# Optimization experiments

Measured on AMD Instinct MI355X. Metric: run time of the kernel, lower is better.

The kernel has to match this reference:

```python
import jax, jax.numpy as jnp
import numpy as np

N = 50000
E = 800000
D_IN = 128
D_OUT = 128


def setup_inputs() -> dict:
    key = jax.random.key(0)
    ks = jax.random.split(key, 12)
    x = jax.random.normal(ks[0], (N, D_IN), dtype=jnp.float32)
    W1 = jax.random.normal(ks[1], (D_IN, D_OUT), dtype=jnp.float32) * (1.0 / np.sqrt(D_IN))
    b1 = jnp.zeros((D_OUT,), dtype=jnp.float32)
    W2 = jax.random.normal(ks[2], (D_IN, D_OUT), dtype=jnp.float32) * (1.0 / np.sqrt(D_IN))
    b2 = jnp.zeros((D_OUT,), dtype=jnp.float32)
    # inverted-dropout masks, p=0.5 -> values in {0, 2}
    def mask(k):
        return jnp.where(jax.random.uniform(k, (N, D_IN)) < 0.5, 0.0, 2.0).astype(jnp.float32)
    mask_pos1 = mask(ks[3])
    mask_neg1 = mask(ks[4])
    mask_pos2 = mask(ks[5])
    mask_neg2 = mask(ks[6])
    edge_index1 = jax.random.randint(ks[7], (2, E), 0, N, dtype=jnp.int32)
    edge_index2 = jax.random.randint(ks[8], (2, E), 0, N, dtype=jnp.int32)
    perm1 = jax.random.permutation(ks[9], N).astype(jnp.int32)
    perm2 = jax.random.permutation(ks[10], N).astype(jnp.int32)
    return dict(x=x, W1=W1, b1=b1, W2=W2, b2=b2,
                mask_pos1=mask_pos1, mask_neg1=mask_neg1,
                mask_pos2=mask_pos2, mask_neg2=mask_neg2,
                edge_index1=edge_index1, edge_index2=edge_index2,
                perm1=perm1, perm2=perm2)


def gcn_conv(x, W, b, edge_index):
    """PyG GCNConv: add self-loops, symmetric normalization, then x@W aggregation + bias."""
    n = x.shape[0]
    xw = x @ W  # [N, D_OUT]
    loops = jnp.arange(n, dtype=edge_index.dtype)
    src = jnp.concatenate([edge_index[0], loops])
    dst = jnp.concatenate([edge_index[1], loops])
    deg = jax.ops.segment_sum(jnp.ones_like(dst, dtype=xw.dtype), dst, num_segments=n)
    dinv = jax.lax.rsqrt(jnp.maximum(deg, 1.0))  # deg >= 1 due to self-loops
    norm = dinv[src] * dinv[dst]                 # [E+N]
    msg = xw[src] * norm[:, None]                # [E+N, D_OUT]
    out = jax.ops.segment_sum(msg, dst, num_segments=n)
    return out + b


def _branch(x, W, b, edge_index, mask_pos, mask_neg, perm):
    pos_h = jax.nn.relu(gcn_conv(x * mask_pos, W, b, edge_index))
    neg_in = (x * mask_neg)[perm]
    neg_h = jax.nn.relu(gcn_conv(neg_in, W, b, edge_index))
    summary = jnp.mean(pos_h, axis=0, keepdims=True)  # [1, D_OUT]
    return pos_h, neg_h, summary


def reference(x, W1, b1, W2, b2, mask_pos1, mask_neg1, mask_pos2, mask_neg2,
              edge_index1, edge_index2, perm1, perm2):
    p1, n1, s1 = _branch(x, W1, b1, edge_index1, mask_pos1, mask_neg1, perm1)
    p2, n2, s2 = _branch(x, W2, b2, edge_index2, mask_pos2, mask_neg2, perm2)
    return (p1, n1, s1, p2, n2, s2)
```

## Files before the change

kernel.cpp:

```cpp
#include <hip/hip_runtime.h>
#include <hip/hip_fp16.h>

#define NN 50000
#define NE 800000
#define D 128
#define NB 196
#define FILL_BLOCKS 1024
#define GEMM_BLOCKS 3128
#define RNG 6250
#define BCAP 131072

typedef _Float16 half8_t __attribute__((ext_vector_type(8)));
typedef _Float16 half4_t __attribute__((ext_vector_type(4)));
typedef float f32x4 __attribute__((ext_vector_type(4)));

__global__ void k_init(int* cnt1, int* cnt2, float* s1, float* s2, int* bcnt) {
    int i = blockIdx.x * blockDim.x + threadIdx.x;
    int stride = gridDim.x * blockDim.x;
    for (int j = i; j < NN; j += stride) { cnt1[j] = 0; cnt2[j] = 0; }
    if (i < D) { s1[i] = 0.f; s2[i] = 0.f; }
    if (i < 16) bcnt[i] = 0;
}

__global__ void k_bucket(const int* __restrict__ src1, const int* __restrict__ dst1,
                         const int* __restrict__ src2, const int* __restrict__ dst2,
                         int* bcnt,
                         int* bs1, int* bd1, int* bs2, int* bd2) {
    __shared__ int lcnt[16], lpos[16], gbase[16];
    int t = threadIdx.x;
    if (t < 16) { lcnt[t] = 0; lpos[t] = 0; }
    __syncthreads();

    int e0 = blockIdx.x * 256 + t;
    int s1v0=0,d1v0=0,s2v0=0,d2v0=0, s1v1=0,d1v1=0,s2v1=0,d2v1=0;
    int s1v2=0,d1v2=0,s2v2=0,d2v2=0, s1v3=0,d1v3=0,s2v3=0,d2v3=0;
    bool v0 = (e0 + 0 * 262144) < NE;
    bool v1 = (e0 + 1 * 262144) < NE;
    bool v2 = (e0 + 2 * 262144) < NE;
    bool v3 = (e0 + 3 * 262144) < NE;
    if (v0) { int e = e0;             s1v0 = src1[e]; d1v0 = dst1[e]; s2v0 = src2[e]; d2v0 = dst2[e]; }
    if (v1) { int e = e0 + 262144;    s1v1 = src1[e]; d1v1 = dst1[e]; s2v1 = src2[e]; d2v1 = dst2[e]; }
    if (v2) { int e = e0 + 2*262144;  s1v2 = src1[e]; d1v2 = dst1[e]; s2v2 = src2[e]; d2v2 = dst2[e]; }
    if (v3) { int e = e0 + 3*262144;  s1v3 = src1[e]; d1v3 = dst1[e]; s2v3 = src2[e]; d2v3 = dst2[e]; }

    if (v0) { atomicAdd(&lcnt[d1v0 / RNG], 1); atomicAdd(&lcnt[8 + d2v0 / RNG], 1); }
    if (v1) { atomicAdd(&lcnt[d1v1 / RNG], 1); atomicAdd(&lcnt[8 + d2v1 / RNG], 1); }
    if (v2) { atomicAdd(&lcnt[d1v2 / RNG], 1); atomicAdd(&lcnt[8 + d2v2 / RNG], 1); }
    if (v3) { atomicAdd(&lcnt[d1v3 / RNG], 1); atomicAdd(&lcnt[8 + d2v3 / RNG], 1); }
    __syncthreads();
    if (t < 16) gbase[t] = atomicAdd(&bcnt[t], lcnt[t]);
    __syncthreads();

    #define PLACE(sv, dv) { \
        int r = (dv) / RNG; \
        int p = gbase[r] + atomicAdd(&lpos[r], 1); \
        if (p < BCAP) { bs1[r * BCAP + p] = (sv); bd1[r * BCAP + p] = (dv); } }
    #define PLACE2(sv, dv) { \
        int r = (dv) / RNG; \
        int p = gbase[8 + r] + atomicAdd(&lpos[8 + r], 1); \
        if (p < BCAP) { bs2[r * BCAP + p] = (sv); bd2[r * BCAP + p] = (dv); } }
    if (v0) { PLACE(s1v0, d1v0); PLACE2(s2v0, d2v0); }
    if (v1) { PLACE(s1v1, d1v1); PLACE2(s2v1, d2v1); }
    if (v2) { PLACE(s1v2, d1v2); PLACE2(s2v2, d2v2); }
    if (v3) { PLACE(s1v3, d1v3); PLACE2(s2v3, d2v3); }
    #undef PLACE
    #undef PLACE2
}

__global__ void k_count_b(const int* __restrict__ bcnt,
                          const int* __restrict__ bd1, const int* __restrict__ bd2,
                          int* cnt1, int* cnt2) {
    int b = blockIdx.x & 7;
    int rank = blockIdx.x >> 3;
    int base = b * BCAP;
    int n1 = bcnt[b], n2 = bcnt[8 + b];
    for (int i = rank * 256 + threadIdx.x; i < n1; i += 32768)
        atomicAdd(&cnt1[bd1[base + i]], 1);
    for (int i = rank * 256 + threadIdx.x; i < n2; i += 32768)
        atomicAdd(&cnt2[bd2[base + i]], 1);
}

__global__ void k_part(const int* __restrict__ cnt1, const int* __restrict__ cnt2,
                       int* part1, int* part2) {
    __shared__ int sm1[256], sm2[256];
    int t = threadIdx.x;
    int idx = blockIdx.x * 256 + t;
    int v1 = (idx < NN) ? cnt1[idx] : 0;
    int v2 = (idx < NN) ? cnt2[idx] : 0;
    sm1[t] = v1; sm2[t] = v2;
    __syncthreads();
    for (int off = 128; off > 0; off >>= 1) {
        if (t < off) { sm1[t] += sm1[t + off]; sm2[t] += sm2[t + off]; }
        __syncthreads();
    }
    if (t == 0) { part1[blockIdx.x] = sm1[0]; part2[blockIdx.x] = sm2[0]; }
}

__global__ void k_scanp(int* part1, int* part2) {
    __shared__ int sm1[256], sm2[256];
    int t = threadIdx.x;
    int v1 = (t < NB) ? part1[t] : 0;
    int v2 = (t < NB) ? part2[t] : 0;
    sm1[t] = v1; sm2[t] = v2;
    __syncthreads();
    for (int off = 1; off < 256; off <<= 1) {
        int a1 = (t >= off) ? sm1[t - off] : 0;
        int a2 = (t >= off) ? sm2[t - off] : 0;
        __syncthreads();
        sm1[t] += a1; sm2[t] += a2;
        __syncthreads();
    }
    if (t < NB) { part1[t] = sm1[t] - v1; part2[t] = sm2[t] - v2; }
}

__global__ void k_apply(const int* __restrict__ cnt1, const int* __restrict__ cnt2,
                        const int* __restrict__ part1, const int* __restrict__ part2,
                        int* rp1, int* rp2, int* cur1, int* cur2,
                        float* dinv1, float* dinv2) {
    __shared__ int sm1[256], sm2[256];
    int b = blockIdx.x, t = threadIdx.x;
    int idx = b * 256 + t;
    int v1 = (idx < NN) ? cnt1[idx] : 0;
    int v2 = (idx < NN) ? cnt2[idx] : 0;
    sm1[t] = v1; sm2[t] = v2;
    __syncthreads();
    for (int off = 1; off < 256; off <<= 1) {
        int a1 = (t >= off) ? sm1[t - off] : 0;
        int a2 = (t >= off) ? sm2[t - off] : 0;
        __syncthreads();
        sm1[t] += a1; sm2[t] += a2;
        __syncthreads();
    }
    int e1 = sm1[t] - v1 + part1[b];
    int e2 = sm2[t] - v2 + part2[b];
    if (idx < NN) {
        rp1[idx] = e1; cur1[idx] = e1; dinv1[idx] = rsqrtf((float)(v1 + 1));
        rp2[idx] = e2; cur2[idx] = e2; dinv2[idx] = rsqrtf((float)(v2 + 1));
    } else if (idx == NN) {
        rp1[NN] = e1; rp2[NN] = e2;
    }
}

__launch_bounds__(256)
__global__ void k_fill_gemm(const int* __restrict__ bcnt,
                            const int* __restrict__ bs1, const int* __restrict__ bd1,
                            const int* __restrict__ bs2, const int* __restrict__ bd2,
                            int* cur1, int* cur2, int* col1, int* col2,
                            const float* __restrict__ x,
                            const float* __restrict__ W1, const float* __restrict__ W2,
                            const float* __restrict__ mp1, const float* __restrict__ mn1,
                            const float* __restrict__ mp2, const float* __restrict__ mn2,
                            const int* __restrict__ perm1, const int* __restrict__ perm2,
                            const float* __restrict__ dinv1, const float* __restrict__ dinv2,
                            _Float16* xwi1, _Float16* xwi2) {
    __shared__ __align__(16) _Float16 WT[128][136];
    int t = threadIdx.x;
    int bid = blockIdx.x;

    if (bid < FILL_BLOCKS) {
        int b = bid & 7;
        int rank = bid >> 3;
        int base = b * BCAP;
        int n1 = bcnt[b], n2 = bcnt[8 + b];
        for (int i = rank * 256 + t; i < n1; i += 32768) {
            int d = bd1[base + i];
            int p = atomicAdd(&cur1[d], 1);
            col1[p] = bs1[base + i];
        }
        for (int i = rank * 256 + t; i < n2; i += 32768) {
            int d = bd2[base + i];
            int p = atomicAdd(&cur2[d], 1);
            col2[p] = bs2[base + i];
        }
        return;
    }

    int g = bid - FILL_BLOCKS;
    int which = g / 782;
    int bx = g - which * 782;
    const float* W = (which < 2) ? W1 : W2;
    const float* mask = (which == 0) ? mp1 : (which == 1) ? mn1 : (which == 2) ? mp2 : mn2;
    const int* perm = (which == 1) ? perm1 : (which == 3) ? perm2 : nullptr;
    const float* dinv = (which < 2) ? dinv1 : dinv2;
    _Float16* out = ((which < 2) ? xwi1 : xwi2) + ((which & 1) ? 128 : 0);

    #pragma unroll
    for (int i = 0; i < 8; i++) {
        int idx = i * 256 + t;
        int j = idx & 127;
        int k0 = (idx >> 7) * 8;
        half8_t h;
        #pragma unroll
        for (int c = 0; c < 8; c++) h[c] = (_Float16)W[(k0 + c) * 128 + j];
        *(half8_t*)(&WT[j][k0]) = h;
    }
    __syncthreads();

    int wave = t >> 6;
    int lane = t & 63;
    int quad = lane >> 4;
    int m = lane & 15;
    int tile = bx * 4 + wave;
    bool active = (tile * 16 < NN);

    f32x4 accs[8];
    if (active) {
        int row = tile * 16 + m;
        int grow = perm ? perm[row] : row;
        const float* xrow = x + (long)grow * D;
        const float* mrow = mask + (long)grow * D;

        half8_t a[4];
        #pragma unroll
        for (int kk = 0; kk < 4; kk++) {
            int k0 = kk * 32 + quad * 8;
            float4 xa = *(const float4*)(xrow + k0);
            float4 xb = *(const float4*)(xrow + k0 + 4);
            float4 ma = *(const float4*)(mrow + k0);
            float4 mb = *(const float4*)(mrow + k0 + 4);
            a[kk][0] = (_Float16)(xa.x * ma.x);
            a[kk][1] = (_Float16)(xa.y * ma.y);
            a[kk][2] = (_Float16)(xa.z * ma.z);
            a[kk][3] = (_Float16)(xa.w * ma.w);
            a[kk][4] = (_Float16)(xb.x * mb.x);
            a[kk][5] = (_Float16)(xb.y * mb.y);
            a[kk][6] = (_Float16)(xb.z * mb.z);
            a[kk][7] = (_Float16)(xb.w * mb.w);
        }

        #pragma unroll
        for (int nt = 0; nt < 8; nt++) {
            f32x4 acc = {0.f, 0.f, 0.f, 0.f};
            #pragma unroll
            for (int kk = 0; kk < 4; kk++) {
                half8_t w = *(const half8_t*)(&WT[nt * 16 + m][kk * 32 + quad * 8]);
                acc = __builtin_amdgcn_mfma_f32_16x16x32_f16(w, a[kk], acc, 0, 0, 0);
            }
            accs[nt] = acc;
        }
    }

    __syncthreads();

    if (active) {
        float ds = dinv[tile * 16 + m];
        _Float16* st = &WT[0][0] + wave * 2176;

        #pragma unroll
        for (int nt = 0; nt < 8; nt++) {
            half4_t h;
            h[0] = (_Float16)(accs[nt][0] * ds);
            h[1] = (_Float16)(accs[nt][1] * ds);
            h[2] = (_Float16)(accs[nt][2] * ds);
            h[3] = (_Float16)(accs[nt][3] * ds);
            *(half4_t*)(st + m * 136 + nt * 16 + quad * 4) = h;
        }
        #pragma unroll
        for (int p = 0; p < 4; p++) {
            int r = lane & 15;
            int cc = (lane >> 4) + p * 4;
            half8_t v = *(const half8_t*)(st + r * 136 + cc * 8);
            *(half8_t*)(out + (long)(tile * 16 + r) * 256 + cc * 8) = v;
        }
    }
}

__launch_bounds__(256)
__global__ void k_agg(const _Float16* __restrict__ xwi1, const _Float16* __restrict__ xwi2,
                      const int* __restrict__ rp1, const int* __restrict__ col1,
                      const float* __restrict__ dinv1,
                      const int* __restrict__ rp2, const int* __restrict__ col2,
                      const float* __restrict__ dinv2,
                      const float* __restrict__ b1, const float* __restrict__ b2,
                      float* out) {
    int g = blockIdx.y;
    const _Float16* xwi = g ? xwi2 : xwi1;
    const int* rp = g ? rp2 : rp1;
    const int* col = g ? col2 : col1;
    const float* dinv = g ? dinv2 : dinv1;
    const float* bias = g ? b2 : b1;
    float* pos_out = out + (g ? 12800128L : 0L);
    float* neg_out = out + (g ? 19200128L : 6400000L);

    int t = threadIdx.x;
    int wave = t >> 6, lane = t & 63;
    int i = blockIdx.x * 4 + wave;
    if (i >= NN) return;
    int j4 = lane * 4;

    half4_t sv = *(const half4_t*)(xwi + (long)i * 256 + j4);
    float a0 = (float)sv[0], a1 = (float)sv[1], a2 = (float)sv[2], a3 = (float)sv[3];
    int e0 = rp[i], e1 = rp[i + 1];
    int e = e0;
    for (; e + 8 <= e1; e += 8) {
        int s0 = col[e + 0], s1 = col[e + 1], s2 = col[e + 2], s3 = col[e + 3];
        int s4 = col[e + 4], s5 = col[e + 5], s6 = col[e + 6], s7 = col[e + 7];
        half4_t v0 = *(const half4_t*)(xwi + (long)s0 * 256 + j4);
        half4_t v1 = *(const half4_t*)(xwi + (long)s1 * 256 + j4);
        half4_t v2 = *(const half4_t*)(xwi + (long)s2 * 256 + j4);
        half4_t v3 = *(const half4_t*)(xwi + (long)s3 * 256 + j4);
        half4_t v4 = *(const half4_t*)(xwi + (long)s4 * 256 + j4);
        half4_t v5 = *(const half4_t*)(xwi + (long)s5 * 256 + j4);
        half4_t v6 = *(const half4_t*)(xwi + (long)s6 * 256 + j4);
        half4_t v7 = *(const half4_t*)(xwi + (long)s7 * 256 + j4);
        a0 += (float)v0[0] + (float)v1[0] + (float)v2[0] + (float)v3[0]
            + (float)v4[0] + (float)v5[0] + (float)v6[0] + (float)v7[0];
        a1 += (float)v0[1] + (float)v1[1] + (float)v2[1] + (float)v3[1]
            + (float)v4[1] + (float)v5[1] + (float)v6[1] + (float)v7[1];
        a2 += (float)v0[2] + (float)v1[2] + (float)v2[2] + (float)v3[2]
            + (float)v4[2] + (float)v5[2] + (float)v6[2] + (float)v7[2];
        a3 += (float)v0[3] + (float)v1[3] + (float)v2[3] + (float)v3[3]
            + (float)v4[3] + (float)v5[3] + (float)v6[3] + (float)v7[3];
    }
    for (; e + 4 <= e1; e += 4) {
        int s0 = col[e + 0], s1 = col[e + 1], s2 = col[e + 2], s3 = col[e + 3];
        half4_t v0 = *(const half4_t*)(xwi + (long)s0 * 256 + j4);
        half4_t v1 = *(const half4_t*)(xwi + (long)s1 * 256 + j4);
        half4_t v2 = *(const half4_t*)(xwi + (long)s2 * 256 + j4);
        half4_t v3 = *(const half4_t*)(xwi + (long)s3 * 256 + j4);
        a0 += (float)v0[0] + (float)v1[0] + (float)v2[0] + (float)v3[0];
        a1 += (float)v0[1] + (float)v1[1] + (float)v2[1] + (float)v3[1];
        a2 += (float)v0[2] + (float)v1[2] + (float)v2[2] + (float)v3[2];
        a3 += (float)v0[3] + (float)v1[3] + (float)v2[3] + (float)v3[3];
    }
    for (; e < e1; e++) {
        int s = col[e];
        half4_t v = *(const half4_t*)(xwi + (long)s * 256 + j4);
        a0 += (float)v[0]; a1 += (float)v[1]; a2 += (float)v[2]; a3 += (float)v[3];
    }
    float di = dinv[i];
    int jj = (lane < 32) ? j4 : (j4 - 128);
    const f32x4* bp = (const f32x4*)(bias + jj);
    f32x4 bv = *bp;
    f32x4 o;
    o[0] = fmaxf(0.f, di * a0 + bv[0]);
    o[1] = fmaxf(0.f, di * a1 + bv[1]);
    o[2] = fmaxf(0.f, di * a2 + bv[2]);
    o[3] = fmaxf(0.f, di * a3 + bv[3]);
    float* dst = ((lane < 32) ? pos_out : neg_out) + (long)i * D + jj;
    __builtin_nontemporal_store(o, (f32x4*)dst);
}

__launch_bounds__(256)
__global__ void k_sum(const float* __restrict__ pos1, const float* __restrict__ pos2,
                      float* s1, float* s2) {
    int g = blockIdx.y;
    const float* pos = g ? pos2 : pos1;
    float* s = g ? s2 : s1;
    int t = threadIdx.x;
    int rg = t >> 5;
    int j = (t & 31) * 4;
    float4 acc = {0.f, 0.f, 0.f, 0.f};
    for (int i = blockIdx.x * 8 + rg; i < NN; i += gridDim.x * 8) {
        float4 v = *(const float4*)(pos + (long)i * D + j);
        acc.x += v.x; acc.y += v.y; acc.z += v.z; acc.w += v.w;
    }
    __shared__ float sm[8][128];
    sm[rg][j + 0] = acc.x;
    sm[rg][j + 1] = acc.y;
    sm[rg][j + 2] = acc.z;
    sm[rg][j + 3] = acc.w;
    __syncthreads();
    if (t < 128) {
        float v = 0.f;
        for (int r = 0; r < 8; r++) v += sm[r][t];
        atomicAdd(&s[t], v * (1.0f / NN));
    }
}

extern "C" void kernel_launch(void* const* d_in, const int* in_sizes, int n_in,
                              void* d_out, int out_size, void* d_ws, size_t ws_size,
                              hipStream_t stream) {
    const float* x   = (const float*)d_in[0];
    const float* W1  = (const float*)d_in[1];
    const float* b1  = (const float*)d_in[2];
    const float* W2  = (const float*)d_in[3];
    const float* b2  = (const float*)d_in[4];
    const float* mp1 = (const float*)d_in[5];
    const float* mn1 = (const float*)d_in[6];
    const float* mp2 = (const float*)d_in[7];
    const float* mn2 = (const float*)d_in[8];
    const int* e1 = (const int*)d_in[9];
    const int* e2 = (const int*)d_in[10];
    const int* perm1 = (const int*)d_in[11];
    const int* perm2 = (const int*)d_in[12];
    const int* src1 = e1;       const int* dst1 = e1 + NE;
    const int* src2 = e2;       const int* dst2 = e2 + NE;
    float* out = (float*)d_out;

    char* w = (char*)d_ws;
    _Float16* xwi1 = (_Float16*)w; w += (size_t)NN * 256 * 2;
    _Float16* xwi2 = (_Float16*)w; w += (size_t)NN * 256 * 2;
    int* cnt1 = (int*)w;  w += (size_t)NN * 4;
    int* cnt2 = (int*)w;  w += (size_t)NN * 4;
    int* cur1 = (int*)w;  w += (size_t)NN * 4;
    int* cur2 = (int*)w;  w += (size_t)NN * 4;
    int* rp1 = (int*)w;   w += (size_t)(NN + 4) * 4;
    int* rp2 = (int*)w;   w += (size_t)(NN + 4) * 4;
    int* col1 = (int*)w;  w += (size_t)NE * 4;
    int* col2 = (int*)w;  w += (size_t)NE * 4;
    float* dinv1 = (float*)w; w += (size_t)NN * 4;
    float* dinv2 = (float*)w; w += (size_t)NN * 4;
    int* part1 = (int*)w; w += (size_t)256 * 4;
    int* part2 = (int*)w; w += (size_t)256 * 4;
    int* bcnt  = (int*)w; w += (size_t)64 * 4;
    int* bs1 = (int*)w;   w += (size_t)8 * BCAP * 4;
    int* bd1 = (int*)w;   w += (size_t)8 * BCAP * 4;
    int* bs2 = (int*)w;   w += (size_t)8 * BCAP * 4;
    int* bd2 = (int*)w;   w += (size_t)8 * BCAP * 4;

    float* s1 = out + 12800000L;
    float* s2 = out + 25600128L;
    const float* pos1 = out;
    const float* pos2 = out + 12800128L;

    k_init<<<dim3(256), 256, 0, stream>>>(cnt1, cnt2, s1, s2, bcnt);
    k_bucket<<<dim3(1024), 256, 0, stream>>>(src1, dst1, src2, dst2, bcnt,
                                             bs1, bd1, bs2, bd2);
    k_count_b<<<dim3(1024), 256, 0, stream>>>(bcnt, bd1, bd2, cnt1, cnt2);
    k_part<<<dim3(NB), 256, 0, stream>>>(cnt1, cnt2, part1, part2);
    k_scanp<<<dim3(1), 256, 0, stream>>>(part1, part2);
    k_apply<<<dim3(NB), 256, 0, stream>>>(cnt1, cnt2, part1, part2,
                                          rp1, rp2, cur1, cur2, dinv1, dinv2);
    k_fill_gemm<<<dim3(FILL_BLOCKS + GEMM_BLOCKS), 256, 0, stream>>>(
        bcnt, bs1, bd1, bs2, bd2, cur1, cur2, col1, col2,
        x, W1, W2, mp1, mn1, mp2, mn2, perm1, perm2, dinv1, dinv2, xwi1, xwi2);
    k_agg<<<dim3(12500, 2), 256, 0, stream>>>(xwi1, xwi2,
                                              rp1, col1, dinv1, rp2, col2, dinv2,
                                              b1, b2, out);
    k_sum<<<dim3(128, 2), 256, 0, stream>>>(pos1, pos2, s1, s2);
}
```

Baseline: 529.6 us.

## Use 64 fine buckets and fuse degree histogram with CSR scan in shared memory

Edges are now bucketed into 64 destination ranges of 782 nodes each instead of 8 ranges. This lets one block per bucket compute the degree histogram in shared memory and scan it locally, using the preceding bucket counts as its base offset. The global count array, its zeroing, and the separate count/partial/scan/apply kernels are removed. The cost is shared-memory atomics and a serial base-offset sum per block. Bucket capacity is lowered to 16384 per bucket, which assumes a roughly uniform distribution of destinations.

```diff
diff --git a/kernel.cpp b/kernel.cpp
--- a/kernel.cpp
+++ b/kernel.cpp
@@ -4,31 +4,29 @@
 #define NN 50000
 #define NE 800000
 #define D 128
-#define NB 196
 #define FILL_BLOCKS 1024
 #define GEMM_BLOCKS 3128
-#define RNG 6250
-#define BCAP 131072
+#define NBKT 64
+#define BW 782
+#define BCAP 16384
 
 typedef _Float16 half8_t __attribute__((ext_vector_type(8)));
 typedef _Float16 half4_t __attribute__((ext_vector_type(4)));
 typedef float f32x4 __attribute__((ext_vector_type(4)));
 
-__global__ void k_init(int* cnt1, int* cnt2, float* s1, float* s2, int* bcnt) {
-    int i = blockIdx.x * blockDim.x + threadIdx.x;
-    int stride = gridDim.x * blockDim.x;
-    for (int j = i; j < NN; j += stride) { cnt1[j] = 0; cnt2[j] = 0; }
+__global__ void k_init(float* s1, float* s2, int* bcnt) {
+    int i = threadIdx.x;
     if (i < D) { s1[i] = 0.f; s2[i] = 0.f; }
-    if (i < 16) bcnt[i] = 0;
+    if (i < 2 * NBKT) bcnt[i] = 0;
 }
 
 __global__ void k_bucket(const int* __restrict__ src1, const int* __restrict__ dst1,
                          const int* __restrict__ src2, const int* __restrict__ dst2,
                          int* bcnt,
                          int* bs1, int* bd1, int* bs2, int* bd2) {
-    __shared__ int lcnt[16], lpos[16], gbase[16];
-    int t = threadIdx.x;
-    if (t < 16) { lcnt[t] = 0; lpos[t] = 0; }
+    __shared__ int lcnt[128], lpos[128], gbase[128];
+    int t = threadIdx.x;
+    if (t < 128) { lcnt[t] = 0; lpos[t] = 0; }
     __syncthreads();
 
     int e0 = blockIdx.x * 256 + t;
@@ -43,21 +41,21 @@
     if (v2) { int e = e0 + 2*262144;  s1v2 = src1[e]; d1v2 = dst1[e]; s2v2 = src2[e]; d2v2 = dst2[e]; }
     if (v3) { int e = e0 + 3*262144;  s1v3 = src1[e]; d1v3 = dst1[e]; s2v3 = src2[e]; d2v3 = dst2[e]; }
 
-    if (v0) { atomicAdd(&lcnt[d1v0 / RNG], 1); atomicAdd(&lcnt[8 + d2v0 / RNG], 1); }
-    if (v1) { atomicAdd(&lcnt[d1v1 / RNG], 1); atomicAdd(&lcnt[8 + d2v1 / RNG], 1); }
-    if (v2) { atomicAdd(&lcnt[d1v2 / RNG], 1); atomicAdd(&lcnt[8 + d2v2 / RNG], 1); }
-    if (v3) { atomicAdd(&lcnt[d1v3 / RNG], 1); atomicAdd(&lcnt[8 + d2v3 / RNG], 1); }
-    __syncthreads();
-    if (t < 16) gbase[t] = atomicAdd(&bcnt[t], lcnt[t]);
+    if (v0) { atomicAdd(&lcnt[d1v0 / BW], 1); atomicAdd(&lcnt[NBKT + d2v0 / BW], 1); }
+    if (v1) { atomicAdd(&lcnt[d1v1 / BW], 1); atomicAdd(&lcnt[NBKT + d2v1 / BW], 1); }
+    if (v2) { atomicAdd(&lcnt[d1v2 / BW], 1); atomicAdd(&lcnt[NBKT + d2v2 / BW], 1); }
+    if (v3) { atomicAdd(&lcnt[d1v3 / BW], 1); atomicAdd(&lcnt[NBKT + d2v3 / BW], 1); }
+    __syncthreads();
+    if (t < 128) gbase[t] = atomicAdd(&bcnt[t], lcnt[t]);
     __syncthreads();
 
     #define PLACE(sv, dv) { \
-        int r = (dv) / RNG; \
+        int r = (dv) / BW; \
         int p = gbase[r] + atomicAdd(&lpos[r], 1); \
         if (p < BCAP) { bs1[r * BCAP + p] = (sv); bd1[r * BCAP + p] = (dv); } }
     #define PLACE2(sv, dv) { \
-        int r = (dv) / RNG; \
-        int p = gbase[8 + r] + atomicAdd(&lpos[8 + r], 1); \
+        int r = (dv) / BW; \
+        int p = gbase[NBKT + r] + atomicAdd(&lpos[NBKT + r], 1); \
         if (p < BCAP) { bs2[r * BCAP + p] = (sv); bd2[r * BCAP + p] = (dv); } }
     if (v0) { PLACE(s1v0, d1v0); PLACE2(s2v0, d2v0); }
     if (v1) { PLACE(s1v1, d1v1); PLACE2(s2v1, d2v1); }
@@ -67,78 +65,53 @@
     #undef PLACE2
 }
 
-__global__ void k_count_b(const int* __restrict__ bcnt,
-                          const int* __restrict__ bd1, const int* __restrict__ bd2,
-                          int* cnt1, int* cnt2) {
-    int b = blockIdx.x & 7;
-    int rank = blockIdx.x >> 3;
-    int base = b * BCAP;
-    int n1 = bcnt[b], n2 = bcnt[8 + b];
-    for (int i = rank * 256 + threadIdx.x; i < n1; i += 32768)
-        atomicAdd(&cnt1[bd1[base + i]], 1);
-    for (int i = rank * 256 + threadIdx.x; i < n2; i += 32768)
-        atomicAdd(&cnt2[bd2[base + i]], 1);
-}
-
-__global__ void k_part(const int* __restrict__ cnt1, const int* __restrict__ cnt2,
-                       int* part1, int* part2) {
-    __shared__ int sm1[256], sm2[256];
-    int t = threadIdx.x;
-    int idx = blockIdx.x * 256 + t;
-    int v1 = (idx < NN) ? cnt1[idx] : 0;
-    int v2 = (idx < NN) ? cnt2[idx] : 0;
-    sm1[t] = v1; sm2[t] = v2;
-    __syncthreads();
-    for (int off = 128; off > 0; off >>= 1) {
-        if (t < off) { sm1[t] += sm1[t + off]; sm2[t] += sm2[t + off]; }
+__global__ void k_hist(const int* __restrict__ bcnt,
+                       const int* __restrict__ bd1, const int* __restrict__ bd2,
+                       int* rp1, int* rp2, int* cur1, int* cur2,
+                       float* dinv1, float* dinv2) {
+    __shared__ int h[1024];
+    __shared__ int tsum[256];
+    __shared__ int tb[64];
+    __shared__ int bbase;
+    int t = threadIdx.x;
+    int g = blockIdx.x >> 6;
+    int f = blockIdx.x & 63;
+    const int* bd = g ? bd2 : bd1;
+    int* rp = g ? rp2 : rp1;
+    int* cur = g ? cur2 : cur1;
+    float* dinv = g ? dinv2 : dinv1;
+    int n = bcnt[g * NBKT + f];
+    if (n > BCAP) n = BCAP;
+
+    h[t] = 0; h[t + 256] = 0; h[t + 512] = 0; h[t + 768] = 0;
+    if (t < NBKT) tb[t] = bcnt[g * NBKT + t];
+    __syncthreads();
+
+    const int* bdf = bd + f * BCAP;
+    for (int i = t; i < n; i += 256) atomicAdd(&h[bdf[i] - f * BW], 1);
+    if (t == 0) { int b = 0; for (int j = 0; j < f; j++) b += tb[j]; bbase = b; }
+    __syncthreads();
+
+    int a0 = h[4*t], a1 = h[4*t+1], a2 = h[4*t+2], a3 = h[4*t+3];
+    int s = a0 + a1 + a2 + a3;
+    tsum[t] = s;
+    __syncthreads();
+    for (int off = 1; off < 256; off <<= 1) {
+        int add = (t >= off) ? tsum[t - off] : 0;
         __syncthreads();
-    }
-    if (t == 0) { part1[blockIdx.x] = sm1[0]; part2[blockIdx.x] = sm2[0]; }
-}
-
-__global__ void k_scanp(int* part1, int* part2) {
-    __shared__ int sm1[256], sm2[256];
-    int t = threadIdx.x;
-    int v1 = (t < NB) ? part1[t] : 0;
-    int v2 = (t < NB) ? part2[t] : 0;
-    sm1[t] = v1; sm2[t] = v2;
-    __syncthreads();
-    for (int off = 1; off < 256; off <<= 1) {
-        int a1 = (t >= off) ? sm1[t - off] : 0;
-        int a2 = (t >= off) ? sm2[t - off] : 0;
+        tsum[t] += add;
         __syncthreads();
-        sm1[t] += a1; sm2[t] += a2;
-        __syncthreads();
-    }
-    if (t < NB) { part1[t] = sm1[t] - v1; part2[t] = sm2[t] - v2; }
-}
-
-__global__ void k_apply(const int* __restrict__ cnt1, const int* __restrict__ cnt2,
-                        const int* __restrict__ part1, const int* __restrict__ part2,
-                        int* rp1, int* rp2, int* cur1, int* cur2,
-                        float* dinv1, float* dinv2) {
-    __shared__ int sm1[256], sm2[256];
-    int b = blockIdx.x, t = threadIdx.x;
-    int idx = b * 256 + t;
-    int v1 = (idx < NN) ? cnt1[idx] : 0;
-    int v2 = (idx < NN) ? cnt2[idx] : 0;
-    sm1[t] = v1; sm2[t] = v2;
-    __syncthreads();
-    for (int off = 1; off < 256; off <<= 1) {
-        int a1 = (t >= off) ? sm1[t - off] : 0;
-        int a2 = (t >= off) ? sm2[t - off] : 0;
-        __syncthreads();
-        sm1[t] += a1; sm2[t] += a2;
-        __syncthreads();
-    }
-    int e1 = sm1[t] - v1 + part1[b];
-    int e2 = sm2[t] - v2 + part2[b];
-    if (idx < NN) {
-        rp1[idx] = e1; cur1[idx] = e1; dinv1[idx] = rsqrtf((float)(v1 + 1));
-        rp2[idx] = e2; cur2[idx] = e2; dinv2[idx] = rsqrtf((float)(v2 + 1));
-    } else if (idx == NN) {
-        rp1[NN] = e1; rp2[NN] = e2;
-    }
+    }
+    int excl = tsum[t] - s + bbase;
+
+    int idx = 4 * t;
+    int gd = f * BW + idx;
+    int e0 = excl, e1 = excl + a0, e2 = excl + a0 + a1, e3 = excl + a0 + a1 + a2;
+    if (idx + 0 < BW && gd + 0 < NN) { rp[gd+0] = e0; cur[gd+0] = e0; dinv[gd+0] = rsqrtf((float)(a0+1)); }
+    if (idx + 1 < BW && gd + 1 < NN) { rp[gd+1] = e1; cur[gd+1] = e1; dinv[gd+1] = rsqrtf((float)(a1+1)); }
+    if (idx + 2 < BW && gd + 2 < NN) { rp[gd+2] = e2; cur[gd+2] = e2; dinv[gd+2] = rsqrtf((float)(a2+1)); }
+    if (idx + 3 < BW && gd + 3 < NN) { rp[gd+3] = e3; cur[gd+3] = e3; dinv[gd+3] = rsqrtf((float)(a3+1)); }
+    if (f == 63 && t == 0) rp[NN] = NE;
 }
 
 __launch_bounds__(256)
@@ -158,16 +131,17 @@
     int bid = blockIdx.x;
 
     if (bid < FILL_BLOCKS) {
-        int b = bid & 7;
-        int rank = bid >> 3;
-        int base = b * BCAP;
-        int n1 = bcnt[b], n2 = bcnt[8 + b];
-        for (int i = rank * 256 + t; i < n1; i += 32768) {
+        int f = (bid & 7) + 8 * ((bid >> 3) & 7);
+        int rank = bid >> 6;
+        int base = f * BCAP;
+        int n1 = bcnt[f];         if (n1 > BCAP) n1 = BCAP;
+        int n2 = bcnt[NBKT + f];  if (n2 > BCAP) n2 = BCAP;
+        for (int i = rank * 256 + t; i < n1; i += 4096) {
             int d = bd1[base + i];
             int p = atomicAdd(&cur1[d], 1);
             col1[p] = bs1[base + i];
         }
-        for (int i = rank * 256 + t; i < n2; i += 32768) {
+        for (int i = rank * 256 + t; i < n2; i += 4096) {
             int d = bd2[base + i];
             int p = atomicAdd(&cur2[d], 1);
             col2[p] = bs2[base + i];
@@ -391,8 +365,6 @@
     char* w = (char*)d_ws;
     _Float16* xwi1 = (_Float16*)w; w += (size_t)NN * 256 * 2;
     _Float16* xwi2 = (_Float16*)w; w += (size_t)NN * 256 * 2;
-    int* cnt1 = (int*)w;  w += (size_t)NN * 4;
-    int* cnt2 = (int*)w;  w += (size_t)NN * 4;
     int* cur1 = (int*)w;  w += (size_t)NN * 4;
     int* cur2 = (int*)w;  w += (size_t)NN * 4;
     int* rp1 = (int*)w;   w += (size_t)(NN + 4) * 4;
@@ -401,26 +373,21 @@
     int* col2 = (int*)w;  w += (size_t)NE * 4;
     float* dinv1 = (float*)w; w += (size_t)NN * 4;
     float* dinv2 = (float*)w; w += (size_t)NN * 4;
-    int* part1 = (int*)w; w += (size_t)256 * 4;
-    int* part2 = (int*)w; w += (size_t)256 * 4;
-    int* bcnt  = (int*)w; w += (size_t)64 * 4;
-    int* bs1 = (int*)w;   w += (size_t)8 * BCAP * 4;
-    int* bd1 = (int*)w;   w += (size_t)8 * BCAP * 4;
-    int* bs2 = (int*)w;   w += (size_t)8 * BCAP * 4;
-    int* bd2 = (int*)w;   w += (size_t)8 * BCAP * 4;
+    int* bcnt  = (int*)w; w += (size_t)128 * 4;
+    int* bs1 = (int*)w;   w += (size_t)NBKT * BCAP * 4;
+    int* bd1 = (int*)w;   w += (size_t)NBKT * BCAP * 4;
+    int* bs2 = (int*)w;   w += (size_t)NBKT * BCAP * 4;
+    int* bd2 = (int*)w;   w += (size_t)NBKT * BCAP * 4;
 
     float* s1 = out + 12800000L;
     float* s2 = out + 25600128L;
     const float* pos1 = out;
     const float* pos2 = out + 12800128L;
 
-    k_init<<<dim3(256), 256, 0, stream>>>(cnt1, cnt2, s1, s2, bcnt);
+    k_init<<<dim3(1), 256, 0, stream>>>(s1, s2, bcnt);
     k_bucket<<<dim3(1024), 256, 0, stream>>>(src1, dst1, src2, dst2, bcnt,
                                              bs1, bd1, bs2, bd2);
-    k_count_b<<<dim3(1024), 256, 0, stream>>>(bcnt, bd1, bd2, cnt1, cnt2);
-    k_part<<<dim3(NB), 256, 0, stream>>>(cnt1, cnt2, part1, part2);
-    k_scanp<<<dim3(1), 256, 0, stream>>>(part1, part2);
-    k_apply<<<dim3(NB), 256, 0, stream>>>(cnt1, cnt2, part1, part2,
+    k_hist<<<dim3(128), 256, 0, stream>>>(bcnt, bd1, bd2,
                                           rp1, rp2, cur1, cur2, dinv1, dinv2);
     k_fill_gemm<<<dim3(FILL_BLOCKS + GEMM_BLOCKS), 256, 0, stream>>>(
         bcnt, bs1, bd1, bs2, bd2, cur1, cur2, col1, col2,
```

New measurement: 475.4 us. 10.2% less time.
